# Performance work log

Hardware: AMD Instinct MI355X
Metric: run time of the kernel (lower is better)

Reference implementation:

```python
import jax, jax.numpy as jnp
import numpy as np

B, V, J, NB, NC = 4096, 778, 16, 10, 45
PARENTS = [0, 0, 1, 2, 0, 4, 5, 0, 7, 8, 0, 10, 11, 0, 13, 14]
TIPS = [745, 317, 444, 556, 673]
REORDER = [0, 13, 14, 15, 16, 1, 2, 3, 17, 4, 5, 6, 18, 10, 11, 12, 19, 7, 8, 9, 20]


def batch_rodrigues(axisang):
    # axisang: [N,3] -> rotation matrices [N,3,3] via quaternion, matching torch code
    angle = jnp.linalg.norm(axisang + 1e-8, axis=1, keepdims=True)
    axis = axisang / angle
    half = 0.5 * angle
    quat = jnp.concatenate([jnp.cos(half), jnp.sin(half) * axis], axis=1)
    quat = quat / jnp.linalg.norm(quat, axis=1, keepdims=True)
    w, x, y, z = quat[:, 0], quat[:, 1], quat[:, 2], quat[:, 3]
    w2, x2, y2, z2 = w * w, x * x, y * y, z * z
    wx, wy, wz = w * x, w * y, w * z
    xy, xz, yz = x * y, x * z, y * z
    rot = jnp.stack([
        w2 + x2 - y2 - z2, 2 * xy - 2 * wz, 2 * wy + 2 * xz,
        2 * wz + 2 * xy, w2 - x2 + y2 - z2, 2 * yz - 2 * wx,
        2 * xz - 2 * wy, 2 * wx + 2 * yz, w2 - x2 - y2 + z2], axis=1)
    return rot.reshape(-1, 3, 3)


def with_zeros(R, t):
    # R: [B,3,3], t: [B,3] -> homogeneous [B,4,4]
    top = jnp.concatenate([R, t[:, :, None]], axis=2)
    bottom = jnp.broadcast_to(jnp.array([0.0, 0.0, 0.0, 1.0], R.dtype), (R.shape[0], 1, 4))
    return jnp.concatenate([top, bottom], axis=1)


def setup_inputs() -> dict:
    key = jax.random.key(0)
    ks = jax.random.split(key, 10)
    th_J_regressor = jax.random.uniform(ks[6], (J, V), dtype=jnp.float32)
    th_J_regressor = th_J_regressor / th_J_regressor.sum(axis=1, keepdims=True)
    th_weights = jax.random.uniform(ks[7], (V, J), dtype=jnp.float32)
    th_weights = th_weights / th_weights.sum(axis=1, keepdims=True)
    return {
        'th_pose_coeffs': 0.3 * jax.random.normal(ks[0], (B, 3 + NC), dtype=jnp.float32),
        'th_betas': jax.random.normal(ks[1], (B, NB), dtype=jnp.float32),
        'th_trans': jax.random.normal(ks[2], (B, 3), dtype=jnp.float32),
        'th_shapedirs': 0.01 * jax.random.normal(ks[3], (V, 3, NB), dtype=jnp.float32),
        'th_posedirs': 0.01 * jax.random.normal(ks[4], (V, 3, 9 * (J - 1)), dtype=jnp.float32),
        'th_v_template': 0.1 * jax.random.normal(ks[5], (V, 3), dtype=jnp.float32),
        'th_J_regressor': th_J_regressor,
        'th_weights': th_weights,
        'th_selected_comps': jax.random.normal(ks[8], (NC, 45), dtype=jnp.float32),
        'th_hands_mean': jnp.zeros((45,), dtype=jnp.float32),  # flat_hand_mean=True
    }


def reference(th_pose_coeffs, th_betas, th_trans, th_shapedirs, th_posedirs,
              th_v_template, th_J_regressor, th_weights, th_selected_comps,
              th_hands_mean):
    b = th_pose_coeffs.shape[0]
    # PCA pose space -> full 45-dim axis-angle hand pose
    full_hand_pose = th_pose_coeffs[:, 3:3 + NC] @ th_selected_comps
    full_pose = jnp.concatenate(
        [th_pose_coeffs[:, :3], th_hands_mean[None] + full_hand_pose], axis=1)  # [B,48]
    rot_mats = batch_rodrigues(full_pose.reshape(-1, 3)).reshape(b, J, 3, 3)
    root_rot = rot_mats[:, 0]
    pose_map = (rot_mats[:, 1:] - jnp.eye(3, dtype=rot_mats.dtype)).reshape(b, 9 * (J - 1))
    v_shaped = jnp.einsum('vdk,bk->bvd', th_shapedirs, th_betas) + th_v_template[None]
    j = jnp.einsum('jv,bvd->bjd', th_J_regressor, v_shaped)  # [B,16,3]
    # pose blendshapes
    v_posed = v_shaped + jnp.einsum('vdp,bp->bvd', th_posedirs, pose_map)
    # kinematic chain (16 joints, fixed tree)
    transforms = [with_zeros(root_rot, j[:, 0])]
    for i in range(1, J):
        p = PARENTS[i]
        local = with_zeros(rot_mats[:, i], j[:, i] - j[:, p])
        transforms.append(jnp.matmul(transforms[p], local))
    results = jnp.stack(transforms, axis=1)  # [B,16,4,4]
    # remove rest-pose joint locations from translations
    j_h = jnp.concatenate([j, jnp.zeros((b, J, 1), j.dtype)], axis=2)
    corr = jnp.einsum('bjmn,bjn->bjm', results, j_h)  # [B,16,4]
    results2 = results - jnp.concatenate(
        [jnp.zeros(results.shape[:3] + (3,), results.dtype), corr[..., None]], axis=3)
    # linear blend skinning
    T = jnp.einsum('bjmn,vj->bvmn', results2, th_weights)  # [B,778,4,4]
    v_posed_h = jnp.concatenate([v_posed, jnp.ones((b, V, 1), v_posed.dtype)], axis=2)
    verts = jnp.einsum('bvmn,bvn->bvm', T, v_posed_h)[..., :3]  # [B,778,3]
    jtr = results[:, :, :3, 3]  # [B,16,3]
    jtr = jnp.concatenate([jtr, verts[:, TIPS]], axis=1)[:, REORDER]  # [B,21,3]
    verts = (verts + th_trans[:, None]) * 1000.0
    jtr = (jtr + th_trans[:, None]) * 1000.0
    return verts, jtr
```

## Files before the change

kernel.cpp:

```cpp
#include <hip/hip_runtime.h>
#include <hip/hip_bf16.h>
#include <cstddef>

#define B_      4096
#define V_      778
#define J_      16
#define NB_     10
#define NC_     45
#define NROWS   2334
#define PM_     135
#define KPW     192
#define NPW     2432
#define LDK     104

typedef __attribute__((ext_vector_type(8))) short short8v;
typedef __attribute__((ext_vector_type(4))) float f32x4;

#define WS_JS   0
#define WS_JT   480
#define WS_A2   1024
#define WS_VP   (WS_A2  + (size_t)B_*192)
#define WS_ACT  (WS_VP  + (size_t)B_*NPW)
#define WS_BT   (WS_ACT + (size_t)B_*96)

__global__ __launch_bounds__(256) void k_prep(const float* __restrict__ jreg,
                                              const float* __restrict__ shd,
                                              const float* __restrict__ pdr,
                                              const float* __restrict__ tmpl,
                                              float* __restrict__ ws,
                                              __hip_bfloat16* __restrict__ BTg)
{
    int bx = blockIdx.x;
    if (bx < NPW) {
        int n = bx, k = threadIdx.x;
        if (k >= KPW) return;
        float v = 0.f;
        if (n < NROWS) {
            if (k < NB_)            v = shd[n * NB_ + k];
            else if (k < NB_ + PM_) v = pdr[(size_t)n * PM_ + (k - NB_)];
        }
        BTg[(size_t)n * KPW + k] = __float2bfloat16(v);
        return;
    }
    int wid  = ((bx - NPW) * 256 + threadIdx.x) >> 6;
    int lane = threadIdx.x & 63;
    if (wid >= 528) return;
    float s = 0.f;
    if (wid < 480) {
        int i = wid / 30, rem = wid % 30, d = rem / 10, k = rem % 10;
        const float* jr = jreg + i * V_;
        for (int v = lane; v < V_; v += 64) s += jr[v] * shd[v*30 + d*10 + k];
    } else {
        int e = wid - 480, i = e / 3, d = e % 3;
        const float* jr = jreg + i * V_;
        for (int v = lane; v < V_; v += 64) s += jr[v] * tmpl[v*3 + d];
    }
    #pragma unroll
    for (int off = 32; off; off >>= 1) s += __shfl_down(s, off, 64);
    if (lane == 0) ws[wid] = s;
}

__global__ __launch_bounds__(256) void k_pose(const float* __restrict__ pc,
                                              const float* __restrict__ betas,
                                              const float* __restrict__ sc,
                                              const float* __restrict__ hm,
                                              const float* __restrict__ trans,
                                              float* __restrict__ ws,
                                              __hip_bfloat16* __restrict__ ACTg,
                                              float* __restrict__ out_jtr)
{
    __shared__ float scs[NC_*45 + 45];
    __shared__ float sR[16 * 144];
    __shared__ float sj[16 * 48];
    const int tid = threadIdx.x;
    for (int i = tid; i < NC_*45 + 45; i += 256)
        scs[i] = (i < NC_*45) ? sc[i] : hm[i - NC_*45];
    __syncthreads();

    {
        int bl = tid >> 4, i = tid & 15;
        int b  = blockIdx.x * 16 + bl;
        const float* pcb = pc + b * 48;
        __hip_bfloat16* act = ACTg + (size_t)b * KPW;

        float a0, a1, a2;
        if (i == 0) { a0 = pcb[0]; a1 = pcb[1]; a2 = pcb[2]; }
        else {
            int col = (i - 1) * 3;
            float s0 = scs[NC_*45 + col], s1 = scs[NC_*45 + col + 1], s2 = scs[NC_*45 + col + 2];
            for (int k = 0; k < NC_; ++k) {
                float p = pcb[3 + k];
                s0 += p * scs[k*45 + col];
                s1 += p * scs[k*45 + col + 1];
                s2 += p * scs[k*45 + col + 2];
            }
            a0 = s0; a1 = s1; a2 = s2;
        }
        float e0 = a0 + 1e-8f, e1 = a1 + 1e-8f, e2 = a2 + 1e-8f;
        float angle = sqrtf(e0*e0 + e1*e1 + e2*e2);
        float inv  = 1.f / angle;
        float half = 0.5f * angle;
        float sh = sinf(half), ch = cosf(half);
        float w = ch, x = sh * a0 * inv, y = sh * a1 * inv, z = sh * a2 * inv;
        float qn = 1.f / sqrtf(w*w + x*x + y*y + z*z);
        w *= qn; x *= qn; y *= qn; z *= qn;
        float w2 = w*w, x2 = x*x, y2 = y*y, z2 = z*z;
        float wx = w*x, wy = w*y, wz = w*z, xy = x*y, xz = x*z, yz = y*z;
        float R[9] = { w2+x2-y2-z2, 2*xy-2*wz,   2*wy+2*xz,
                       2*wz+2*xy,   w2-x2+y2-z2, 2*yz-2*wx,
                       2*xz-2*wy,   2*wx+2*yz,   w2-x2-y2+z2 };
        #pragma unroll
        for (int q = 0; q < 9; ++q) sR[bl*144 + i*9 + q] = R[q];

        if (i == 0) {
            const float* bb = betas + b * NB_;
            #pragma unroll
            for (int k = 0; k < NB_; ++k) act[k] = __float2bfloat16(bb[k]);
            for (int k = NB_ + PM_; k < KPW; ++k) act[k] = __float2bfloat16(0.f);
        } else {
            #pragma unroll
            for (int q = 0; q < 9; ++q) {
                float pv = R[q] - ((q == 0 || q == 4 || q == 8) ? 1.f : 0.f);
                act[NB_ + (i-1)*9 + q] = __float2bfloat16(pv);
            }
        }
        const float* bb = betas + b * NB_;
        #pragma unroll
        for (int d = 0; d < 3; ++d) {
            const float* jsrow = ws + WS_JS + (i*3 + d) * NB_;
            float s = ws[WS_JT + i*3 + d];
            #pragma unroll
            for (int k = 0; k < NB_; ++k) s += jsrow[k] * bb[k];
            sj[bl*48 + i*3 + d] = s;
        }
    }
    __syncthreads();

    if (tid >= 240) return;
    int bl = tid / 15, rem = tid % 15, f = rem / 3, m = rem % 3;
    int b  = blockIdx.x * 16 + bl;
    const float* rot = &sR[bl * 144];
    const float* j   = &sj[bl * 48];
    float* a2 = ws + WS_A2 + (size_t)b*192;
    float* jt = out_jtr + (size_t)b*63;
    const int INV[16] = {0,5,6,7,9,10,11,17,18,19,13,14,15,1,2,3};
    float trm = trans[b*3 + m];

    float j0x = j[0], j0y = j[1], j0z = j[2];
    float T0 = rot[m*3+0], T1 = rot[m*3+1], T2 = rot[m*3+2];
    float T3 = (m == 0) ? j0x : (m == 1) ? j0y : j0z;
    if (f == 0) {
        float corr = T0*j0x + T1*j0y + T2*j0z;
        a2[m*4+0] = T0; a2[m*4+1] = T1; a2[m*4+2] = T2; a2[m*4+3] = T3 - corr;
        jt[m] = (T3 + trm) * 1000.f;
    }
    float jpx = j0x, jpy = j0y, jpz = j0z;
    for (int s = 0; s < 3; ++s) {
        int i = f*3 + 1 + s;
        const float* R = rot + i*9;
        float jix = j[i*3], jiy = j[i*3+1], jiz = j[i*3+2];
        float d0 = jix - jpx, d1 = jiy - jpy, d2 = jiz - jpz;
        float n0 = T0*R[0] + T1*R[3] + T2*R[6];
        float n1 = T0*R[1] + T1*R[4] + T2*R[7];
        float n2 = T0*R[2] + T1*R[5] + T2*R[8];
        float n3 = T0*d0 + T1*d1 + T2*d2 + T3;
        T0 = n0; T1 = n1; T2 = n2; T3 = n3;
        float corr = T0*jix + T1*jiy + T2*jiz;
        a2[i*12 + m*4 + 0] = T0; a2[i*12 + m*4 + 1] = T1;
        a2[i*12 + m*4 + 2] = T2; a2[i*12 + m*4 + 3] = T3 - corr;
        jt[INV[i]*3 + m] = (T3 + trm) * 1000.f;
        jpx = jix; jpy = jiy; jpz = jiz;
    }
}

__global__ __launch_bounds__(256) void k_mfma(const __hip_bfloat16* __restrict__ ACTg,
                                              const __hip_bfloat16* __restrict__ BTg,
                                              const float* __restrict__ tmpl,
                                              float* __restrict__ vp)
{
    __shared__ ushort lA[128 * LDK];
    __shared__ ushort lB[128 * LDK];

    const int tid  = threadIdx.x;
    const int lane = tid & 63;
    const int wid  = tid >> 6;
    const int wm   = wid >> 1;
    const int wn   = wid & 1;
    const int b0   = blockIdx.y * 128;
    const int n0   = blockIdx.x * 128;
    const int l15  = lane & 15;
    const int lhi  = lane >> 4;

    f32x4 acc[4][4] = {};

    for (int kc = 0; kc < KPW; kc += 96) {
        #pragma unroll
        for (int it = 0; it < 6; ++it) {
            int idx = it * 256 + tid;
            int row = idx / 12, ch = idx % 12;
            const uint4* sa = (const uint4*)(ACTg + (size_t)(b0 + row) * KPW + kc + ch*8);
            *(uint4*)&lA[row*LDK + ch*8] = *sa;
            const uint4* sb = (const uint4*)(BTg + (size_t)(n0 + row) * KPW + kc + ch*8);
            *(uint4*)&lB[row*LDK + ch*8] = *sb;
        }
        __syncthreads();
        #pragma unroll
        for (int ks = 0; ks < 3; ++ks) {
            int kl = ks*32 + lhi*8;
            short8v a[4], bf[4];
            #pragma unroll
            for (int mt = 0; mt < 4; ++mt)
                a[mt] = *(const short8v*)&lA[(wm*64 + mt*16 + l15)*LDK + kl];
            #pragma unroll
            for (int nt = 0; nt < 4; ++nt)
                bf[nt] = *(const short8v*)&lB[(wn*64 + nt*16 + l15)*LDK + kl];
            #pragma unroll
            for (int mt = 0; mt < 4; ++mt)
                #pragma unroll
                for (int nt = 0; nt < 4; ++nt)
                    acc[mt][nt] = __builtin_amdgcn_mfma_f32_16x16x32_bf16(
                        a[mt], bf[nt], acc[mt][nt], 0, 0, 0);
        }
        __syncthreads();
    }
    #pragma unroll
    for (int nt = 0; nt < 4; ++nt) {
        int col = n0 + wn*64 + nt*16 + l15;
        float tv = (col < NROWS) ? tmpl[col] : 0.f;
        #pragma unroll
        for (int mt = 0; mt < 4; ++mt) {
            int rbase = b0 + wm*64 + mt*16 + lhi*4;
            #pragma unroll
            for (int r = 0; r < 4; ++r)
                vp[(size_t)(rbase + r) * NPW + col] = acc[mt][nt][r] + tv;
        }
    }
}

__global__ __launch_bounds__(256) void k_blend3(const float* __restrict__ wts,
                                                const float* __restrict__ trans,
                                                const float* __restrict__ ws,
                                                float* __restrict__ out)
{
    __shared__ float s_wt[16 * 64];
    __shared__ float s_a2[4 * 192];
    __shared__ float s_vp[4 * 192];
    const int tid = threadIdx.x;
    const int v0  = blockIdx.x * 64;
    const int b0  = blockIdx.y * 4;
    const int bl  = tid >> 6;
    const int vl  = tid & 63;
    const int b   = b0 + bl;
    const int v   = v0 + vl;

    {
        int vv = tid >> 2, q = tid & 3;
        int gv = v0 + vv;
        float4 wv = (gv < V_) ? *(const float4*)(wts + gv*16 + q*4)
                              : make_float4(0.f, 0.f, 0.f, 0.f);
        s_wt[(q*4+0)*64 + vv] = wv.x;
        s_wt[(q*4+1)*64 + vv] = wv.y;
        s_wt[(q*4+2)*64 + vv] = wv.z;
        s_wt[(q*4+3)*64 + vv] = wv.w;
    }
    if (tid < 192) {
        int bg = tid / 48, i = tid % 48;
        *(float4*)&s_a2[bg*192 + i*4] =
            *(const float4*)(ws + WS_A2 + (size_t)(b0 + bg)*192 + i*4);
        *(float4*)&s_vp[bg*192 + i*4] =
            *(const float4*)(ws + WS_VP + (size_t)(b0 + bg)*NPW + v0*3 + i*4);
    }
    __syncthreads();

    const float* a2r = &s_a2[bl * 192];
    float T[12] = {};
    #pragma unroll
    for (int jj = 0; jj < 16; ++jj) {
        float wj = s_wt[jj*64 + vl];
        float4 x0 = *(const float4*)&a2r[jj*12];
        float4 x1 = *(const float4*)&a2r[jj*12 + 4];
        float4 x2 = *(const float4*)&a2r[jj*12 + 8];
        T[0] += wj*x0.x; T[1] += wj*x0.y; T[2]  += wj*x0.z; T[3]  += wj*x0.w;
        T[4] += wj*x1.x; T[5] += wj*x1.y; T[6]  += wj*x1.z; T[7]  += wj*x1.w;
        T[8] += wj*x2.x; T[9] += wj*x2.y; T[10] += wj*x2.z; T[11] += wj*x2.w;
    }
    float p0 = s_vp[bl*192 + vl*3];
    float p1 = s_vp[bl*192 + vl*3 + 1];
    float p2 = s_vp[bl*192 + vl*3 + 2];
    float o0 = T[0]*p0 + T[1]*p1 + T[2]*p2  + T[3];
    float o1 = T[4]*p0 + T[5]*p1 + T[6]*p2  + T[7];
    float o2 = T[8]*p0 + T[9]*p1 + T[10]*p2 + T[11];

    float t0 = trans[b*3], t1 = trans[b*3+1], t2 = trans[b*3+2];
    float r0 = (o0 + t0)*1000.f, r1 = (o1 + t1)*1000.f, r2 = (o2 + t2)*1000.f;

    if (v < V_) {
        float* vo = out + (size_t)b*NROWS + v*3;
        vo[0] = r0; vo[1] = r1; vo[2] = r2;
        const int TIPS[5] = {745, 317, 444, 556, 673};
        const int TIPK[5] = {4, 8, 12, 16, 20};
        #pragma unroll
        for (int t = 0; t < 5; ++t) {
            if (v == TIPS[t]) {
                float* jt = out + (size_t)B_*NROWS + (size_t)b*63 + TIPK[t]*3;
                jt[0] = r0; jt[1] = r1; jt[2] = r2;
            }
        }
    }
}

extern "C" void kernel_launch(void* const* d_in, const int* in_sizes, int n_in,
                              void* d_out, int out_size, void* d_ws, size_t ws_size,
                              hipStream_t stream)
{
    const float* pc    = (const float*)d_in[0];
    const float* betas = (const float*)d_in[1];
    const float* trans = (const float*)d_in[2];
    const float* shd   = (const float*)d_in[3];
    const float* pdr   = (const float*)d_in[4];
    const float* tmpl  = (const float*)d_in[5];
    const float* jreg  = (const float*)d_in[6];
    const float* wts   = (const float*)d_in[7];
    const float* sc    = (const float*)d_in[8];
    const float* hm    = (const float*)d_in[9];
    float* out = (float*)d_out;
    float* ws  = (float*)d_ws;

    __hip_bfloat16* ACTg = (__hip_bfloat16*)(ws + WS_ACT);
    __hip_bfloat16* BTg  = (__hip_bfloat16*)(ws + WS_BT);
    float* vp = ws + WS_VP;

    hipLaunchKernelGGL(k_prep,   dim3(NPW + 132), dim3(256), 0, stream,
                       jreg, shd, pdr, tmpl, ws, BTg);
    hipLaunchKernelGGL(k_pose,   dim3(B_/16),     dim3(256), 0, stream,
                       pc, betas, sc, hm, trans, ws, ACTg,
                       out + (size_t)B_ * NROWS);
    hipLaunchKernelGGL(k_mfma,   dim3(19, 32),    dim3(256), 0, stream, ACTg, BTg, tmpl, vp);
    hipLaunchKernelGGL(k_blend3, dim3(13, B_/4),  dim3(256), 0, stream, wts, trans, ws, out);
}
```

Before: 144.4 us.

## Store posed vertices as bf16 and loop vertex tiles inside blend kernel

The matmul epilogue now writes the posed-vertex intermediate in bf16 rather than fp32, which halves that workspace traffic. The blend kernel becomes one block per four batches that loops over all 13 vertex tiles, so the a2 transforms and translations are loaded once per block. The cost is reduced precision in the posed vertices, since the template offset is added before rounding, and fewer, longer blocks that reload the weight tile on each iteration.

```diff
diff --git a/kernel.cpp b/kernel.cpp
--- a/kernel.cpp
+++ b/kernel.cpp
@@ -19,8 +19,8 @@
 #define WS_JS   0
 #define WS_JT   480
 #define WS_A2   1024
-#define WS_VP   (WS_A2  + (size_t)B_*192)
-#define WS_ACT  (WS_VP  + (size_t)B_*NPW)
+#define WS_VPH  (WS_A2  + (size_t)B_*192)
+#define WS_ACT  (WS_VPH + (size_t)B_*NPW/2)
 #define WS_BT   (WS_ACT + (size_t)B_*96)
 
 __global__ __launch_bounds__(256) void k_prep(const float* __restrict__ jreg,
@@ -176,7 +176,7 @@
 __global__ __launch_bounds__(256) void k_mfma(const __hip_bfloat16* __restrict__ ACTg,
                                               const __hip_bfloat16* __restrict__ BTg,
                                               const float* __restrict__ tmpl,
-                                              float* __restrict__ vp)
+                                              __hip_bfloat16* __restrict__ vph)
 {
     __shared__ ushort lA[128 * LDK];
     __shared__ ushort lB[128 * LDK];
@@ -232,78 +232,88 @@
             int rbase = b0 + wm*64 + mt*16 + lhi*4;
             #pragma unroll
             for (int r = 0; r < 4; ++r)
-                vp[(size_t)(rbase + r) * NPW + col] = acc[mt][nt][r] + tv;
-        }
-    }
-}
-
-__global__ __launch_bounds__(256) void k_blend3(const float* __restrict__ wts,
+                vph[(size_t)(rbase + r) * NPW + col] =
+                    __float2bfloat16(acc[mt][nt][r] + tv);
+        }
+    }
+}
+
+__global__ __launch_bounds__(256) void k_blend4(const float* __restrict__ wts,
                                                 const float* __restrict__ trans,
                                                 const float* __restrict__ ws,
+                                                const __hip_bfloat16* __restrict__ vph,
                                                 float* __restrict__ out)
 {
+    __shared__ float s_a2[4 * 192];
     __shared__ float s_wt[16 * 64];
-    __shared__ float s_a2[4 * 192];
-    __shared__ float s_vp[4 * 192];
+    __shared__ __hip_bfloat16 s_vp[4 * 192];
     const int tid = threadIdx.x;
-    const int v0  = blockIdx.x * 64;
-    const int b0  = blockIdx.y * 4;
+    const int b0  = blockIdx.x * 4;
     const int bl  = tid >> 6;
     const int vl  = tid & 63;
     const int b   = b0 + bl;
-    const int v   = v0 + vl;
-
-    {
-        int vv = tid >> 2, q = tid & 3;
-        int gv = v0 + vv;
-        float4 wv = (gv < V_) ? *(const float4*)(wts + gv*16 + q*4)
-                              : make_float4(0.f, 0.f, 0.f, 0.f);
-        s_wt[(q*4+0)*64 + vv] = wv.x;
-        s_wt[(q*4+1)*64 + vv] = wv.y;
-        s_wt[(q*4+2)*64 + vv] = wv.z;
-        s_wt[(q*4+3)*64 + vv] = wv.w;
-    }
+
     if (tid < 192) {
         int bg = tid / 48, i = tid % 48;
         *(float4*)&s_a2[bg*192 + i*4] =
             *(const float4*)(ws + WS_A2 + (size_t)(b0 + bg)*192 + i*4);
-        *(float4*)&s_vp[bg*192 + i*4] =
-            *(const float4*)(ws + WS_VP + (size_t)(b0 + bg)*NPW + v0*3 + i*4);
-    }
-    __syncthreads();
-
+    }
+    float t0 = trans[b*3], t1 = trans[b*3+1], t2 = trans[b*3+2];
     const float* a2r = &s_a2[bl * 192];
-    float T[12] = {};
-    #pragma unroll
-    for (int jj = 0; jj < 16; ++jj) {
-        float wj = s_wt[jj*64 + vl];
-        float4 x0 = *(const float4*)&a2r[jj*12];
-        float4 x1 = *(const float4*)&a2r[jj*12 + 4];
-        float4 x2 = *(const float4*)&a2r[jj*12 + 8];
-        T[0] += wj*x0.x; T[1] += wj*x0.y; T[2]  += wj*x0.z; T[3]  += wj*x0.w;
-        T[4] += wj*x1.x; T[5] += wj*x1.y; T[6]  += wj*x1.z; T[7]  += wj*x1.w;
-        T[8] += wj*x2.x; T[9] += wj*x2.y; T[10] += wj*x2.z; T[11] += wj*x2.w;
-    }
-    float p0 = s_vp[bl*192 + vl*3];
-    float p1 = s_vp[bl*192 + vl*3 + 1];
-    float p2 = s_vp[bl*192 + vl*3 + 2];
-    float o0 = T[0]*p0 + T[1]*p1 + T[2]*p2  + T[3];
-    float o1 = T[4]*p0 + T[5]*p1 + T[6]*p2  + T[7];
-    float o2 = T[8]*p0 + T[9]*p1 + T[10]*p2 + T[11];
-
-    float t0 = trans[b*3], t1 = trans[b*3+1], t2 = trans[b*3+2];
-    float r0 = (o0 + t0)*1000.f, r1 = (o1 + t1)*1000.f, r2 = (o2 + t2)*1000.f;
-
-    if (v < V_) {
-        float* vo = out + (size_t)b*NROWS + v*3;
-        vo[0] = r0; vo[1] = r1; vo[2] = r2;
-        const int TIPS[5] = {745, 317, 444, 556, 673};
-        const int TIPK[5] = {4, 8, 12, 16, 20};
-        #pragma unroll
-        for (int t = 0; t < 5; ++t) {
-            if (v == TIPS[t]) {
-                float* jt = out + (size_t)B_*NROWS + (size_t)b*63 + TIPK[t]*3;
-                jt[0] = r0; jt[1] = r1; jt[2] = r2;
+    const int TIPS[5] = {745, 317, 444, 556, 673};
+    const int TIPK[5] = {4, 8, 12, 16, 20};
+
+    for (int vt = 0; vt < 13; ++vt) {
+        const int v0 = vt * 64;
+        __syncthreads();
+        {
+            int vv = tid >> 2, q = tid & 3;
+            int gv = v0 + vv;
+            float4 wv = (gv < V_) ? *(const float4*)(wts + gv*16 + q*4)
+                                  : make_float4(0.f, 0.f, 0.f, 0.f);
+            s_wt[(q*4+0)*64 + vv] = wv.x;
+            s_wt[(q*4+1)*64 + vv] = wv.y;
+            s_wt[(q*4+2)*64 + vv] = wv.z;
+            s_wt[(q*4+3)*64 + vv] = wv.w;
+        }
+        if (tid < 192) {
+            int bg = tid / 48, i = tid % 48;
+            int off = v0*3 + i*4;
+            if (off + 3 < NPW)
+                *(uint2*)&s_vp[bg*192 + i*4] =
+                    *(const uint2*)(vph + (size_t)(b0 + bg)*NPW + off);
+        }
+        __syncthreads();
+
+        int v = v0 + vl;
+        float T[12] = {};
+        #pragma unroll
+        for (int jj = 0; jj < 16; ++jj) {
+            float wj = s_wt[jj*64 + vl];
+            float4 x0 = *(const float4*)&a2r[jj*12];
+            float4 x1 = *(const float4*)&a2r[jj*12 + 4];
+            float4 x2 = *(const float4*)&a2r[jj*12 + 8];
+            T[0] += wj*x0.x; T[1] += wj*x0.y; T[2]  += wj*x0.z; T[3]  += wj*x0.w;
+            T[4] += wj*x1.x; T[5] += wj*x1.y; T[6]  += wj*x1.z; T[7]  += wj*x1.w;
+            T[8] += wj*x2.x; T[9] += wj*x2.y; T[10] += wj*x2.z; T[11] += wj*x2.w;
+        }
+        float p0 = __bfloat162float(s_vp[bl*192 + vl*3]);
+        float p1 = __bfloat162float(s_vp[bl*192 + vl*3 + 1]);
+        float p2 = __bfloat162float(s_vp[bl*192 + vl*3 + 2]);
+        float o0 = T[0]*p0 + T[1]*p1 + T[2]*p2  + T[3];
+        float o1 = T[4]*p0 + T[5]*p1 + T[6]*p2  + T[7];
+        float o2 = T[8]*p0 + T[9]*p1 + T[10]*p2 + T[11];
+        float r0 = (o0 + t0)*1000.f, r1 = (o1 + t1)*1000.f, r2 = (o2 + t2)*1000.f;
+
+        if (v < V_) {
+            float* vo = out + (size_t)b*NROWS + v*3;
+            vo[0] = r0; vo[1] = r1; vo[2] = r2;
+            #pragma unroll
+            for (int t = 0; t < 5; ++t) {
+                if (v == TIPS[t]) {
+                    float* jt = out + (size_t)B_*NROWS + (size_t)b*63 + TIPK[t]*3;
+                    jt[0] = r0; jt[1] = r1; jt[2] = r2;
+                }
             }
         }
     }
@@ -328,13 +338,13 @@
 
     __hip_bfloat16* ACTg = (__hip_bfloat16*)(ws + WS_ACT);
     __hip_bfloat16* BTg  = (__hip_bfloat16*)(ws + WS_BT);
-    float* vp = ws + WS_VP;
+    __hip_bfloat16* vph  = (__hip_bfloat16*)(ws + WS_VPH);
 
     hipLaunchKernelGGL(k_prep,   dim3(NPW + 132), dim3(256), 0, stream,
                        jreg, shd, pdr, tmpl, ws, BTg);
     hipLaunchKernelGGL(k_pose,   dim3(B_/16),     dim3(256), 0, stream,
                        pc, betas, sc, hm, trans, ws, ACTg,
                        out + (size_t)B_ * NROWS);
-    hipLaunchKernelGGL(k_mfma,   dim3(19, 32),    dim3(256), 0, stream, ACTg, BTg, tmpl, vp);
-    hipLaunchKernelGGL(k_blend3, dim3(13, B_/4),  dim3(256), 0, stream, wts, trans, ws, out);
-}
+    hipLaunchKernelGGL(k_mfma,   dim3(19, 32),    dim3(256), 0, stream, ACTg, BTg, tmpl, vph);
+    hipLaunchKernelGGL(k_blend4, dim3(B_/4),      dim3(256), 0, stream, wts, trans, ws, vph, out);
+}
```

After: 153.9 us. 1.07x slower.
